# Kernel optimization log

Hardware: AMD Instinct MI355X
Metric: run time of the kernel (lower is better)

## Reference

```python
import jax, jax.numpy as jnp
import numpy as np

B, C, S, H, W = 8, 64, 64, 128, 128
HID = 32           # max(C//2, 8)
STEPS, DT, OMEGA_MAX = 10, 0.3, 2.0
EPS = 1e-5


def _dw(x, k):
    # depthwise 3x3 conv, NCHW, kernel [C,1,3,3]
    return jax.lax.conv_general_dilated(
        x, k, (1, 1), 'SAME',
        dimension_numbers=('NCHW', 'OIHW', 'NCHW'),
        feature_group_count=x.shape[1])


def _pw(x, w, b=None):
    # pointwise (1x1) conv as einsum, w: [out,in]
    y = jnp.einsum('bihw,oi->bohw', x, w)
    return y if b is None else y + b[None, :, None, None]


def _lrelu(x):
    return jax.nn.leaky_relu(x, 0.2)


def setup_inputs() -> dict:
    key = jax.random.key(0)
    ks = jax.random.split(key, 16)
    d = {
        'force': jax.random.normal(ks[0], (B, C, H, W), jnp.float32),
        'style': jax.random.normal(ks[1], (1, S, 1, 1), jnp.float32),
        'illum_feat': jax.random.normal(ks[2], (B, C, H, W), jnp.float32),
        # HyperEncoder 1x1 convs
        'h_w1': 0.05 * jax.random.normal(ks[3], (HID, C + S), jnp.float32),
        'h_b1': jnp.zeros((HID,), jnp.float32),
        'h_w2': 0.05 * jax.random.normal(ks[4], (HID, HID), jnp.float32),
        'h_b2': jnp.zeros((HID,), jnp.float32),
        'h_w3': 0.05 * jax.random.normal(ks[5], (4 * C, HID), jnp.float32),
        'h_b3': jnp.zeros((4 * C,), jnp.float32),
        # OscillatorCell convs (no bias)
        'dw_k': 0.05 * jax.random.normal(ks[6], (C, 1, 3, 3), jnp.float32),
        'pw_w': 0.05 * jax.random.normal(ks[7], (C, C), jnp.float32),
        # refine: dw3x3 (+bias), pw, lrelu, pw
        'r_dw_k': 0.05 * jax.random.normal(ks[8], (C, 1, 3, 3), jnp.float32),
        'r_dw_b': jnp.zeros((C,), jnp.float32),
        'r_pw1_w': 0.05 * jax.random.normal(ks[9], (C, C), jnp.float32),
        'r_pw1_b': jnp.zeros((C,), jnp.float32),
        'r_pw2_w': 0.05 * jax.random.normal(ks[10], (C, C), jnp.float32),
        'r_pw2_b': jnp.zeros((C,), jnp.float32),
        'layer_scale': 0.01 * jnp.ones((1, C, 1, 1), jnp.float32),
    }
    return d


def reference(force, style, illum_feat,
              h_w1, h_b1, h_w2, h_b2, h_w3, h_b3,
              dw_k, pw_w,
              r_dw_k, r_dw_b, r_pw1_w, r_pw1_b, r_pw2_w, r_pw2_b,
              layer_scale):
    force = force + 0.2 * illum_feat
    b, c, h, w = force.shape

    # HyperEncoder
    style_map = jnp.broadcast_to(style, (b, style.shape[1], h, w))
    u = jnp.concatenate([force, style_map], axis=1)
    u = _lrelu(_pw(u, h_w1, h_b1))
    u = _lrelu(_pw(u, h_w2, h_b2))
    p = _pw(u, h_w3, h_b3)
    wch, zch, gch, bch = jnp.split(p, 4, axis=1)
    omega = jax.nn.sigmoid(wch) * OMEGA_MAX
    zeta = jax.nn.sigmoid(zch)
    gamma = jax.nn.sigmoid(gch) * 2.0
    beta = jnp.tanh(bch)

    # unrolled symplectic-Euler oscillator recurrence
    def step(carry, _):
        x, v = carry
        coupling = _dw(x, dw_k) + _pw(x, pw_w)
        accel = force + coupling - 2.0 * zeta * omega * v - omega ** 2 * x
        v = v + accel * DT
        x = x + v * DT
        return (x, v), None

    x0 = jnp.zeros_like(force)
    (x, v), _ = jax.lax.scan(step, (x0, x0), None, length=STEPS)

    # instance norm (no affine) + style modulation
    fx = force + x
    mu = fx.mean(axis=(2, 3), keepdims=True)
    var = fx.var(axis=(2, 3), keepdims=True)
    out = gamma * ((fx - mu) / jnp.sqrt(var + EPS)) + beta

    # refine branch with layer scale
    r = _dw(out, r_dw_k) + r_dw_b[None, :, None, None]
    r = _lrelu(_pw(r, r_pw1_w, r_pw1_b))
    r = _pw(r, r_pw2_w, r_pw2_b)
    out = out + layer_scale * r
    return (out, x, v)
```

## Files before the change

### kernel.cpp

```cpp
#include <hip/hip_runtime.h>
#include <hip/hip_fp16.h>

#define Hn 128
#define Wn 128
#define HWn 16384
#define Cn 64
#define Bn 8
#define NTOT (Bn*Cn*HWn)
#define NPIX (Bn*HWn)
#define DTc 0.3f
#define EPSc 1e-5f

__device__ __forceinline__ float sigm(float t){ return 1.0f/(1.0f+__expf(-t)); }

__global__ void fuseF0(const float4* __restrict__ force, const float4* __restrict__ illum,
                       __half* __restrict__ F, __half* __restrict__ XA, __half* __restrict__ V)
{
    int i = blockIdx.x * blockDim.x + threadIdx.x;
    float4 f = force[i], il = illum[i];
    float a0 = f.x + 0.2f*il.x, a1 = f.y + 0.2f*il.y;
    float a2 = f.z + 0.2f*il.z, a3 = f.w + 0.2f*il.w;
    uint2 pf, px, pv;
    __half2 h;
    h = __floats2half2_rn(a0, a1);            pf.x = *(unsigned int*)&h;
    h = __floats2half2_rn(a2, a3);            pf.y = *(unsigned int*)&h;
    h = __floats2half2_rn(0.09f*a0, 0.09f*a1); px.x = *(unsigned int*)&h;
    h = __floats2half2_rn(0.09f*a2, 0.09f*a3); px.y = *(unsigned int*)&h;
    h = __floats2half2_rn(0.3f*a0, 0.3f*a1);   pv.x = *(unsigned int*)&h;
    h = __floats2half2_rn(0.3f*a2, 0.3f*a3);   pv.y = *(unsigned int*)&h;
    *reinterpret_cast<uint2*>(F  + 4*(size_t)i) = pf;
    *reinterpret_cast<uint2*>(XA + 4*(size_t)i) = px;
    *reinterpret_cast<uint2*>(V  + 4*(size_t)i) = pv;
}

__global__ void prep(const float* __restrict__ style, const float* __restrict__ w1,
                     const float* __restrict__ b1, const float* __restrict__ pw,
                     const float* __restrict__ pw1, const float* __restrict__ pw2,
                     float* __restrict__ w1T, float* __restrict__ c1,
                     float* __restrict__ pwT, float* __restrict__ pw1T,
                     float* __restrict__ pw2T)
{
    int t = threadIdx.x;
    if (t < 32) {
        float s = b1[t];
        for (int k = 0; k < 64; k++) s += w1[t*128 + 64 + k] * style[k];
        c1[t] = s;
    }
    for (int i = t; i < 2048; i += 256) { int c = i >> 5, j = i & 31; w1T[i] = w1[j*128 + c]; }
    for (int i = t; i < 4096; i += 256) {
        int c = i >> 6, k = i & 63;
        pwT[i]  = pw[k*64 + c];
        pw1T[i] = pw1[k*64 + c];
        pw2T[i] = pw2[k*64 + c];
    }
}

__global__ void hyper2(const __half* __restrict__ F,
                       const float* __restrict__ w1T, const float* __restrict__ c1,
                       const float* __restrict__ w2, const float* __restrict__ b2,
                       const float* __restrict__ w3, const float* __restrict__ b3,
                       __half2* __restrict__ AB, __half2* __restrict__ GB)
{
    int p = blockIdx.x * blockDim.x + threadIdx.x;
    int b  = p >> 14;
    int sp = p & (HWn - 1);
    int base = b * Cn * HWn + sp;

    float u1[32];
#pragma unroll
    for (int j = 0; j < 32; j++) u1[j] = c1[j];
#pragma unroll 4
    for (int c = 0; c < 64; c++) {
        float fc = __half2float(F[base + c*HWn]);
        const float* __restrict__ wr = w1T + c*32;
#pragma unroll
        for (int j = 0; j < 32; j++) u1[j] += wr[j] * fc;
    }
#pragma unroll
    for (int j = 0; j < 32; j++) { float v = u1[j]; u1[j] = v > 0.f ? v : 0.2f*v; }

    float u2[32];
#pragma unroll
    for (int i = 0; i < 32; i++) {
        float s = b2[i];
#pragma unroll
        for (int j = 0; j < 32; j++) s += w2[i*32 + j] * u1[j];
        u2[i] = s > 0.f ? s : 0.2f*s;
    }

    if (blockIdx.y == 0) {
        for (int j = 0; j < 64; j++) {
            const float* __restrict__ r0 = w3 + j*32;
            const float* __restrict__ r1 = w3 + (64 + j)*32;
            float pwv = b3[j], pz = b3[64 + j];
#pragma unroll
            for (int i = 0; i < 32; i++) { pwv += r0[i]*u2[i]; pz += r1[i]*u2[i]; }
            float om = 2.0f * sigm(pwv);
            float ze = sigm(pz);
            AB[base + j*HWn] = __floats2half2_rn(2.0f * ze * om, om * om);
        }
    } else {
        for (int j = 0; j < 64; j++) {
            const float* __restrict__ r2 = w3 + (128 + j)*32;
            const float* __restrict__ r3 = w3 + (192 + j)*32;
            float pg = b3[128 + j], pb = b3[192 + j];
#pragma unroll
            for (int i = 0; i < 32; i++) { pg += r2[i]*u2[i]; pb += r3[i]*u2[i]; }
            GB[base + j*HWn] = __floats2half2_rn(2.0f * sigm(pg), tanhf(pb));
        }
    }
}

template <bool LAST>
__global__ void osc_step(const __half* __restrict__ Xin, __half* __restrict__ Xout,
                         __half* __restrict__ V, const __half* __restrict__ F,
                         const __half2* __restrict__ AB,
                         const float* __restrict__ dwk, const float* __restrict__ pwT,
                         float* __restrict__ Xf, float* __restrict__ Vf)
{
    int p = blockIdx.x * blockDim.x + threadIdx.x;
    int c0 = blockIdx.y << 4;
    int b  = p >> 14;
    int sp = p & (HWn - 1);
    int y = sp >> 7, x = sp & 127;
    int base = b * Cn * HWn + sp;

    float acc[16];
#pragma unroll
    for (int k = 0; k < 16; k++) acc[k] = 0.f;
#pragma unroll 4
    for (int c = 0; c < 64; c++) {
        float xc = __half2float(Xin[base + c*HWn]);
        const float* __restrict__ wr = pwT + c*64 + c0;
#pragma unroll
        for (int k = 0; k < 16; k++) acc[k] += wr[k] * xc;
    }

    int   yo[3] = { y > 0 ? -Wn : 0, 0, y < Hn-1 ? Wn : 0 };
    int   xo[3] = { x > 0 ? -1  : 0, 0, x < Wn-1 ? 1  : 0 };
    float my[3] = { y > 0 ? 1.f : 0.f, 1.f, y < Hn-1 ? 1.f : 0.f };
    float mx[3] = { x > 0 ? 1.f : 0.f, 1.f, x < Wn-1 ? 1.f : 0.f };
    float mm[9]; int oo[9];
#pragma unroll
    for (int dy = 0; dy < 3; dy++)
#pragma unroll
        for (int dx = 0; dx < 3; dx++) { mm[dy*3+dx] = my[dy]*mx[dx]; oo[dy*3+dx] = yo[dy]+xo[dx]; }

#pragma unroll
    for (int cc = 0; cc < 16; cc++) {
        int c = c0 + cc;
        int cb = base + c*HWn;
        float tv[9];
#pragma unroll
        for (int t = 0; t < 9; t++) tv[t] = __half2float(Xin[cb + oo[t]]);
        float dws = 0.f;
#pragma unroll
        for (int t = 0; t < 9; t++) dws += (dwk[c*9 + t] * mm[t]) * tv[t];
        float xc = tv[4];
        float2 ab = __half22float2(AB[cb]);
        float vv = __half2float(V[cb]);
        float accel = __half2float(F[cb]) + acc[cc] + dws - ab.x * vv - ab.y * xc;
        vv += accel * DTc;
        float xn = xc + vv * DTc;
        if constexpr (!LAST) {
            V[cb] = __float2half(vv);
            Xout[cb] = __float2half(xn);
        } else {
            Xf[cb] = xn;
            Vf[cb] = vv;
        }
    }
}

__global__ void inorm_stats(const __half* __restrict__ F, const float* __restrict__ X,
                            float* __restrict__ mu, float* __restrict__ rs)
{
    int bc = blockIdx.x;
    int base = bc * HWn;
    const __half2* __restrict__ F2 = (const __half2*)(F + base);
    const float4*  __restrict__ X4 = (const float4*)(X + base);
    float s = 0.f, s2 = 0.f;
    for (int i = threadIdx.x; i < HWn/4; i += blockDim.x) {
        float4 xv = X4[i];
        float2 f0 = __half22float2(F2[2*i]);
        float2 f1 = __half22float2(F2[2*i+1]);
        float v0 = f0.x + xv.x, v1 = f0.y + xv.y, v2 = f1.x + xv.z, v3 = f1.y + xv.w;
        s += (v0 + v1) + (v2 + v3);
        s2 += (v0*v0 + v1*v1) + (v2*v2 + v3*v3);
    }
#pragma unroll
    for (int o = 32; o > 0; o >>= 1) { s += __shfl_down(s, o); s2 += __shfl_down(s2, o); }
    __shared__ float sh[16];
    int w = threadIdx.x >> 6, l = threadIdx.x & 63;
    if (l == 0) { sh[w] = s; sh[8 + w] = s2; }
    __syncthreads();
    if (threadIdx.x == 0) {
        float S = 0.f, S2 = 0.f;
        for (int i = 0; i < 4; i++) { S += sh[i]; S2 += sh[8 + i]; }
        float m = S / (float)HWn;
        float var = S2 / (float)HWn - m*m;
        mu[bc] = m;
        rs[bc] = rsqrtf(var + EPSc);
    }
}

__global__ void modulate(const __half* __restrict__ F, const float4* __restrict__ X4,
                         const uint4* __restrict__ GBu, const float* __restrict__ mu,
                         const float* __restrict__ rs, __half* __restrict__ outp)
{
    int e4 = blockIdx.x * blockDim.x + threadIdx.x;
    int bc = e4 >> 12;
    float m = mu[bc], r = rs[bc];
    uint2 fu = *reinterpret_cast<const uint2*>(F + 4*(size_t)e4);
    float2 f0 = __half22float2(*(__half2*)&fu.x);
    float2 f1 = __half22float2(*(__half2*)&fu.y);
    float4 xv = X4[e4];
    uint4 gb = GBu[e4];
    float2 g0 = __half22float2(*(__half2*)&gb.x);
    float2 g1 = __half22float2(*(__half2*)&gb.y);
    float2 g2 = __half22float2(*(__half2*)&gb.z);
    float2 g3 = __half22float2(*(__half2*)&gb.w);
    float o0 = g0.x * ((f0.x + xv.x - m) * r) + g0.y;
    float o1 = g1.x * ((f0.y + xv.y - m) * r) + g1.y;
    float o2 = g2.x * ((f1.x + xv.z - m) * r) + g2.y;
    float o3 = g3.x * ((f1.y + xv.w - m) * r) + g3.y;
    __half2 h01 = __floats2half2_rn(o0, o1);
    __half2 h23 = __floats2half2_rn(o2, o3);
    uint2 pack; pack.x = *(unsigned int*)&h01; pack.y = *(unsigned int*)&h23;
    *reinterpret_cast<uint2*>(outp + 4*(size_t)e4) = pack;
}

__global__ __launch_bounds__(512)
void refine(const __half* __restrict__ outp,
            const float* __restrict__ rdwk, const float* __restrict__ rdwb,
            const float* __restrict__ pw1T, const float* __restrict__ pb1,
            const float* __restrict__ pw2T, const float* __restrict__ pb2,
            const float* __restrict__ ls, float* __restrict__ out)
{
    __shared__ unsigned int rv2_s[64][64];
    __shared__ unsigned int act2_s[64][64];
    __shared__ __half w1s[64][64];
    __shared__ __half w2s[64][64];
    __shared__ float  dwks[576];
    __shared__ __half2 pb1h[32], pb2h[32];
    __shared__ float  rdwbs[64], lss[64];
    int t = threadIdx.x;
    for (int i = t; i < 4096; i += 512) {
        w1s[i>>6][i&63] = __float2half(pw1T[i]);
        w2s[i>>6][i&63] = __float2half(pw2T[i]);
    }
    for (int i = t; i < 576; i += 512) dwks[i] = rdwk[i];
    if (t < 64) { rdwbs[t]=rdwb[t]; lss[t]=ls[t]; }
    if (t < 32) {
        pb1h[t] = __floats2half2_rn(pb1[2*t], pb1[2*t+1]);
        pb2h[t] = __floats2half2_rn(pb2[2*t], pb2[2*t+1]);
    }

    int l  = t & 63;
    int g  = t >> 6;
    int c0 = g << 3;
    int row = blockIdx.x;
    int b = row >> 7, y = row & 127;
    int base = b * Cn * HWn + y * Wn;
    int px0 = l << 1;

    int   yo[3] = { y > 0 ? -Wn : 0, 0, y < Hn-1 ? Wn : 0 };
    float my[3] = { y > 0 ? 1.f : 0.f, 1.f, y < Hn-1 ? 1.f : 0.f };
    float wl = l > 0  ? 1.f : 0.f;
    float wr = l < 63 ? 1.f : 0.f;
    int loff = l > 0 ? -1 : 0;
    __syncthreads();

#pragma unroll
    for (int cc = 0; cc < 8; cc++) {
        int c = c0 + cc;
        int cb = base + c*HWn + px0;
        float rv0 = rdwbs[c], rv1 = rdwbs[c];
#pragma unroll
        for (int r = 0; r < 3; r++) {
            const __half* __restrict__ rp = outp + cb + yo[r];
            unsigned int cu = *reinterpret_cast<const unsigned int*>(rp);
            float2 ct = __half22float2(*(__half2*)&cu);
            float lf = __half2float(rp[loff]);
            float rt = __half2float(rp[2]);
            float k0 = dwks[c*9 + r*3 + 0] * my[r];
            float k1 = dwks[c*9 + r*3 + 1] * my[r];
            float k2 = dwks[c*9 + r*3 + 2] * my[r];
            rv0 += k0*(wl*lf) + k1*ct.x + k2*ct.y;
            rv1 += k0*ct.x + k1*ct.y + k2*(wr*rt);
        }
        __half2 hv = __floats2half2_rn(rv0, rv1);
        rv2_s[c][l] = *(unsigned int*)&hv;
    }
    __syncthreads();

    __half2 accA[4], accB[4];
#pragma unroll
    for (int q = 0; q < 4; q++) { accA[q] = pb1h[(c0 >> 1) + q]; accB[q] = accA[q]; }
#pragma unroll 8
    for (int c = 0; c < 64; c++) {
        unsigned int rvu = rv2_s[c][l];
        __half2 rvp = *(__half2*)&rvu;
        __half2 r0 = __half2half2(__low2half(rvp));
        __half2 r1 = __half2half2(__high2half(rvp));
        uint4 wq = *reinterpret_cast<const uint4*>(&w1s[c][c0]);
        __half2 w01 = *(__half2*)&wq.x, w23 = *(__half2*)&wq.y;
        __half2 w45 = *(__half2*)&wq.z, w67 = *(__half2*)&wq.w;
        accA[0] = __hfma2(w01, r0, accA[0]); accB[0] = __hfma2(w01, r1, accB[0]);
        accA[1] = __hfma2(w23, r0, accA[1]); accB[1] = __hfma2(w23, r1, accB[1]);
        accA[2] = __hfma2(w45, r0, accA[2]); accB[2] = __hfma2(w45, r1, accB[2]);
        accA[3] = __hfma2(w67, r0, accA[3]); accB[3] = __hfma2(w67, r1, accB[3]);
    }
#pragma unroll
    for (int q = 0; q < 4; q++) {
        float2 a0 = __half22float2(accA[q]);
        float2 a1 = __half22float2(accB[q]);
        float e0 = a0.x > 0.f ? a0.x : 0.2f*a0.x;
        float e1 = a0.y > 0.f ? a0.y : 0.2f*a0.y;
        float e2 = a1.x > 0.f ? a1.x : 0.2f*a1.x;
        float e3 = a1.y > 0.f ? a1.y : 0.2f*a1.y;
        __half2 p0 = __floats2half2_rn(e0, e2);
        __half2 p1 = __floats2half2_rn(e1, e3);
        act2_s[c0 + 2*q][l]     = *(unsigned int*)&p0;
        act2_s[c0 + 2*q + 1][l] = *(unsigned int*)&p1;
    }
    __syncthreads();

#pragma unroll
    for (int q = 0; q < 4; q++) { accA[q] = pb2h[(c0 >> 1) + q]; accB[q] = accA[q]; }
#pragma unroll 8
    for (int j = 0; j < 64; j++) {
        unsigned int au = act2_s[j][l];
        __half2 ap = *(__half2*)&au;
        __half2 a0 = __half2half2(__low2half(ap));
        __half2 a1 = __half2half2(__high2half(ap));
        uint4 wq = *reinterpret_cast<const uint4*>(&w2s[j][c0]);
        __half2 w01 = *(__half2*)&wq.x, w23 = *(__half2*)&wq.y;
        __half2 w45 = *(__half2*)&wq.z, w67 = *(__half2*)&wq.w;
        accA[0] = __hfma2(w01, a0, accA[0]); accB[0] = __hfma2(w01, a1, accB[0]);
        accA[1] = __hfma2(w23, a0, accA[1]); accB[1] = __hfma2(w23, a1, accB[1]);
        accA[2] = __hfma2(w45, a0, accA[2]); accB[2] = __hfma2(w45, a1, accB[2]);
        accA[3] = __hfma2(w67, a0, accA[3]); accB[3] = __hfma2(w67, a1, accB[3]);
    }
#pragma unroll
    for (int q = 0; q < 4; q++) {
        float2 a0 = __half22float2(accA[q]);
        float2 a1 = __half22float2(accB[q]);
        int ca = c0 + 2*q, cb2 = ca + 1;
        int ba = base + ca*HWn + px0;
        int bb = base + cb2*HWn + px0;
        unsigned int oua = *reinterpret_cast<const unsigned int*>(outp + ba);
        unsigned int oub = *reinterpret_cast<const unsigned int*>(outp + bb);
        float2 oa = __half22float2(*(__half2*)&oua);
        float2 ob = __half22float2(*(__half2*)&oub);
        float la = lss[ca], lb = lss[cb2];
        *reinterpret_cast<float2*>(out + ba) = make_float2(oa.x + la*a0.x, oa.y + la*a1.x);
        *reinterpret_cast<float2*>(out + bb) = make_float2(ob.x + lb*a0.y, ob.y + lb*a1.y);
    }
}

extern "C" void kernel_launch(void* const* d_in, const int* in_sizes, int n_in,
                              void* d_out, int out_size, void* d_ws, size_t ws_size,
                              hipStream_t stream)
{
    (void)in_sizes; (void)n_in; (void)out_size; (void)ws_size;
    const float* force   = (const float*)d_in[0];
    const float* style   = (const float*)d_in[1];
    const float* illum   = (const float*)d_in[2];
    const float* h_w1    = (const float*)d_in[3];
    const float* h_b1    = (const float*)d_in[4];
    const float* h_w2    = (const float*)d_in[5];
    const float* h_b2    = (const float*)d_in[6];
    const float* h_w3    = (const float*)d_in[7];
    const float* h_b3    = (const float*)d_in[8];
    const float* dw_k    = (const float*)d_in[9];
    const float* pw_w    = (const float*)d_in[10];
    const float* r_dw_k  = (const float*)d_in[11];
    const float* r_dw_b  = (const float*)d_in[12];
    const float* r_pw1_w = (const float*)d_in[13];
    const float* r_pw1_b = (const float*)d_in[14];
    const float* r_pw2_w = (const float*)d_in[15];
    const float* r_pw2_b = (const float*)d_in[16];
    const float* lscale  = (const float*)d_in[17];

    float* out  = (float*)d_out;
    float* Xf32 = out + (size_t)NTOT;
    float* Vf32 = out + 2*(size_t)NTOT;
    __half2* GB = (__half2*)out;

    char* w = (char*)d_ws;
    __half2* AB = (__half2*)w; w += (size_t)NTOT*4;
    __half*  F  = (__half*)w;  w += (size_t)NTOT*2;
    __half*  XA = (__half*)w;  w += (size_t)NTOT*2;
    __half*  XB = (__half*)w;  w += (size_t)NTOT*2;
    __half*  Vh = (__half*)w;  w += (size_t)NTOT*2;
    float* w1T  = (float*)w;
    float* c1   = w1T + 2048;
    float* pwT  = c1 + 32;
    float* pw1T = pwT + 4096;
    float* pw2T = pw1T + 4096;
    float* mu   = pw2T + 4096;
    float* rs   = mu + 512;
    __half* outp = (__half*)AB;

    fuseF0<<<NTOT/1024, 256, 0, stream>>>((const float4*)force, (const float4*)illum,
                                          F, XA, Vh);
    prep<<<1, 256, 0, stream>>>(style, h_w1, h_b1, pw_w, r_pw1_w, r_pw2_w,
                                w1T, c1, pwT, pw1T, pw2T);
    hyper2<<<dim3(NPIX/256, 2), 256, 0, stream>>>(F, w1T, c1, h_w2, h_b2, h_w3, h_b3,
                                                  AB, GB);
    for (int s = 1; s <= 8; s++) {
        const __half* xin = (s & 1) ? XA : XB;
        __half*      xout = (s & 1) ? XB : XA;
        osc_step<false><<<dim3(NPIX/256, 4), 256, 0, stream>>>(xin, xout, Vh, F, AB,
                                                               dw_k, pwT, nullptr, nullptr);
    }
    osc_step<true><<<dim3(NPIX/256, 4), 256, 0, stream>>>(XA, XB, Vh, F, AB,
                                                          dw_k, pwT, Xf32, Vf32);
    inorm_stats<<<Bn*Cn, 256, 0, stream>>>(F, Xf32, mu, rs);
    modulate<<<NTOT/1024, 256, 0, stream>>>(F, (const float4*)Xf32,
                                            (const uint4*)GB, mu, rs, outp);
    refine<<<NPIX/128, 512, 0, stream>>>(outp, r_dw_k, r_dw_b, pw1T, r_pw1_b,
                                         pw2T, r_pw2_b, lscale, out);
}
```

Measured before the change: 508.7 us.

## Merge hyper encoder halves with packed half2 FMA and remap oscillator block order

The hyper encoder no longer launches two y-blocks that each recompute the first two layers. A single pass now computes all four output heads using packed half2 weights prepared in prep and __hfma2 accumulation. The oscillator step grid is flattened and remapped so that the four channel-group blocks for the same pixel chunk are scheduled near each other, which should improve L2 reuse of the Xin reads. Half-precision accumulation in the last hyper layer lowers accuracy.

New measurement: 495.1 us. 1.03x faster.

```diff
diff --git a/kernel.cpp b/kernel.cpp
--- a/kernel.cpp
+++ b/kernel.cpp
@@ -36,9 +36,12 @@
 __global__ void prep(const float* __restrict__ style, const float* __restrict__ w1,
                      const float* __restrict__ b1, const float* __restrict__ pw,
                      const float* __restrict__ pw1, const float* __restrict__ pw2,
+                     const float* __restrict__ w3, const float* __restrict__ b3,
                      float* __restrict__ w1T, float* __restrict__ c1,
                      float* __restrict__ pwT, float* __restrict__ pw1T,
-                     float* __restrict__ pw2T)
+                     float* __restrict__ pw2T,
+                     __half2* __restrict__ w3abP, __half2* __restrict__ w3gbP,
+                     __half2* __restrict__ b3abP, __half2* __restrict__ b3gbP)
 {
     int t = threadIdx.x;
     if (t < 32) {
@@ -53,12 +56,22 @@
         pw1T[i] = pw1[k*64 + c];
         pw2T[i] = pw2[k*64 + c];
     }
-}
-
-__global__ void hyper2(const __half* __restrict__ F,
+    for (int i = t; i < 2048; i += 256) {
+        int j = i >> 5, k = i & 31;
+        w3abP[i] = __floats2half2_rn(w3[j*32 + k],         w3[(64 + j)*32 + k]);
+        w3gbP[i] = __floats2half2_rn(w3[(128 + j)*32 + k], w3[(192 + j)*32 + k]);
+    }
+    if (t < 64) {
+        b3abP[t] = __floats2half2_rn(b3[t],       b3[64 + t]);
+        b3gbP[t] = __floats2half2_rn(b3[128 + t], b3[192 + t]);
+    }
+}
+
+__global__ void hyperM(const __half* __restrict__ F,
                        const float* __restrict__ w1T, const float* __restrict__ c1,
                        const float* __restrict__ w2, const float* __restrict__ b2,
-                       const float* __restrict__ w3, const float* __restrict__ b3,
+                       const __half2* __restrict__ w3abP, const __half2* __restrict__ w3gbP,
+                       const __half2* __restrict__ b3abP, const __half2* __restrict__ b3gbP,
                        __half2* __restrict__ AB, __half2* __restrict__ GB)
 {
     int p = blockIdx.x * blockDim.x + threadIdx.x;
@@ -87,27 +100,27 @@
         for (int j = 0; j < 32; j++) s += w2[i*32 + j] * u1[j];
         u2[i] = s > 0.f ? s : 0.2f*s;
     }
-
-    if (blockIdx.y == 0) {
-        for (int j = 0; j < 64; j++) {
-            const float* __restrict__ r0 = w3 + j*32;
-            const float* __restrict__ r1 = w3 + (64 + j)*32;
-            float pwv = b3[j], pz = b3[64 + j];
-#pragma unroll
-            for (int i = 0; i < 32; i++) { pwv += r0[i]*u2[i]; pz += r1[i]*u2[i]; }
-            float om = 2.0f * sigm(pwv);
-            float ze = sigm(pz);
-            AB[base + j*HWn] = __floats2half2_rn(2.0f * ze * om, om * om);
+    __half2 u2b[32];
+#pragma unroll
+    for (int i = 0; i < 32; i++) u2b[i] = __half2half2(__float2half(u2[i]));
+
+#pragma unroll 2
+    for (int j = 0; j < 64; j++) {
+        __half2 aab = b3abP[j];
+        __half2 agb = b3gbP[j];
+        const __half2* __restrict__ wa = w3abP + j*32;
+        const __half2* __restrict__ wg = w3gbP + j*32;
+#pragma unroll
+        for (int i = 0; i < 32; i++) {
+            aab = __hfma2(wa[i], u2b[i], aab);
+            agb = __hfma2(wg[i], u2b[i], agb);
         }
-    } else {
-        for (int j = 0; j < 64; j++) {
-            const float* __restrict__ r2 = w3 + (128 + j)*32;
-            const float* __restrict__ r3 = w3 + (192 + j)*32;
-            float pg = b3[128 + j], pb = b3[192 + j];
-#pragma unroll
-            for (int i = 0; i < 32; i++) { pg += r2[i]*u2[i]; pb += r3[i]*u2[i]; }
-            GB[base + j*HWn] = __floats2half2_rn(2.0f * sigm(pg), tanhf(pb));
-        }
+        float2 tab = __half22float2(aab);
+        float om = 2.0f * sigm(tab.x);
+        float ze = sigm(tab.y);
+        AB[base + j*HWn] = __floats2half2_rn(2.0f * ze * om, om * om);
+        float2 tgb = __half22float2(agb);
+        GB[base + j*HWn] = __floats2half2_rn(2.0f * sigm(tgb.x), tanhf(tgb.y));
     }
 }
 
@@ -118,8 +131,11 @@
                          const float* __restrict__ dwk, const float* __restrict__ pwT,
                          float* __restrict__ Xf, float* __restrict__ Vf)
 {
-    int p = blockIdx.x * blockDim.x + threadIdx.x;
-    int c0 = blockIdx.y << 4;
+    int wid  = blockIdx.x;
+    int slot = wid >> 3;
+    int pc   = ((wid & 7) << 6) + (slot >> 2);
+    int c0   = (slot & 3) << 4;
+    int p = (pc << 8) + threadIdx.x;
     int b  = p >> 14;
     int sp = p & (HWn - 1);
     int y = sp >> 7, x = sp & 127;
@@ -401,22 +417,26 @@
     float* pw2T = pw1T + 4096;
     float* mu   = pw2T + 4096;
     float* rs   = mu + 512;
+    __half2* w3abP = (__half2*)(rs + 512);
+    __half2* w3gbP = w3abP + 2048;
+    __half2* b3abP = w3gbP + 2048;
+    __half2* b3gbP = b3abP + 64;
     __half* outp = (__half*)AB;
 
     fuseF0<<<NTOT/1024, 256, 0, stream>>>((const float4*)force, (const float4*)illum,
                                           F, XA, Vh);
-    prep<<<1, 256, 0, stream>>>(style, h_w1, h_b1, pw_w, r_pw1_w, r_pw2_w,
-                                w1T, c1, pwT, pw1T, pw2T);
-    hyper2<<<dim3(NPIX/256, 2), 256, 0, stream>>>(F, w1T, c1, h_w2, h_b2, h_w3, h_b3,
-                                                  AB, GB);
+    prep<<<1, 256, 0, stream>>>(style, h_w1, h_b1, pw_w, r_pw1_w, r_pw2_w, h_w3, h_b3,
+                                w1T, c1, pwT, pw1T, pw2T, w3abP, w3gbP, b3abP, b3gbP);
+    hyperM<<<NPIX/256, 256, 0, stream>>>(F, w1T, c1, h_w2, h_b2,
+                                         w3abP, w3gbP, b3abP, b3gbP, AB, GB);
     for (int s = 1; s <= 8; s++) {
         const __half* xin = (s & 1) ? XA : XB;
         __half*      xout = (s & 1) ? XB : XA;
-        osc_step<false><<<dim3(NPIX/256, 4), 256, 0, stream>>>(xin, xout, Vh, F, AB,
-                                                               dw_k, pwT, nullptr, nullptr);
-    }
-    osc_step<true><<<dim3(NPIX/256, 4), 256, 0, stream>>>(XA, XB, Vh, F, AB,
-                                                          dw_k, pwT, Xf32, Vf32);
+        osc_step<false><<<2048, 256, 0, stream>>>(xin, xout, Vh, F, AB,
+                                                  dw_k, pwT, nullptr, nullptr);
+    }
+    osc_step<true><<<2048, 256, 0, stream>>>(XA, XB, Vh, F, AB,
+                                             dw_k, pwT, Xf32, Vf32);
     inorm_stats<<<Bn*Cn, 256, 0, stream>>>(F, Xf32, mu, rs);
     modulate<<<NTOT/1024, 256, 0, stream>>>(F, (const float4*)Xf32,
                                             (const uint4*)GB, mu, rs, outp);
```
